# Performance work log

Hardware: AMD Instinct MI355X
Metric: run time of the kernel (lower is better)

## Reference

```python
import jax, jax.numpy as jnp
import numpy as np

B, N, D, P = 4, 512, 512, 128

def setup_inputs() -> dict:
    key = jax.random.key(0)
    ks = jax.random.split(key, 8)
    s = lambda fan_in: 1.0 / np.sqrt(fan_in)
    inp = {
        "input": jax.random.normal(ks[0], (B, N, D), dtype=jnp.float32),
        # bigram projections (weights stored [in, out]; torch Linear is [out, in])
        "Wl": jax.random.uniform(ks[1], (D, P), jnp.float32, -s(D), s(D)),
        "bl": jnp.zeros((P,), jnp.float32),  # zeroed in initialize_parameters
        "Wr": jax.random.uniform(ks[2], (D, P), jnp.float32, -s(D), s(D)),  # no bias
        "Wo": jax.random.uniform(ks[3], (P, 1), jnp.float32, -s(P), s(P)),
        "bo": jnp.zeros((1,), jnp.float32),
        # start builder MLP
        "Ws1": jax.random.uniform(ks[4], (D, P), jnp.float32, -s(D), s(D)),
        "bs1": jnp.zeros((P,), jnp.float32),
        "Ws2": jax.random.uniform(ks[5], (P, 1), jnp.float32, -s(P), s(P)),
        "bs2": jnp.zeros((1,), jnp.float32),
        # end builder MLP
        "We1": jax.random.uniform(ks[6], (D, P), jnp.float32, -s(D), s(D)),
        "be1": jnp.zeros((P,), jnp.float32),
        "We2": jax.random.uniform(ks[7], (P, 1), jnp.float32, -s(P), s(P)),
        "be2": jnp.zeros((1,), jnp.float32),
    }
    return inp


def reference(input, Wl, bl, Wr, Wo, bo, Ws1, bs1, Ws2, bs2, We1, be1, We2, be2):
    # start / end unigram scores: [B, N, 1]
    start = jnp.maximum(input @ Ws1 + bs1, 0.0) @ Ws2 + bs2
    end = jnp.maximum(input @ We1 + be1, 0.0) @ We2 + be2
    # bigram scores
    left = input @ Wl + bl   # [B, N, P]
    right = input @ Wr       # [B, N, P]
    # left.unsqueeze(1) + right.unsqueeze(2) -> [B, N, N, P]
    proj = left[:, None, :, :] + right[:, :, None, :]
    bigram = jnp.maximum(proj, 0.0) @ Wo + bo  # [B, N, N, 1]
    return (bigram, start, end)
```

## Files before the change

### kernel.cpp

```cpp
#include <hip/hip_runtime.h>

typedef unsigned short ushort_t;
using f32x4  = __attribute__((ext_vector_type(4))) float;
using bf16x8 = __attribute__((ext_vector_type(8))) short;
using u16x8  = __attribute__((ext_vector_type(8))) unsigned short;
using h2v    = __attribute__((ext_vector_type(2))) _Float16;
using u32x4  = __attribute__((ext_vector_type(4))) unsigned;

constexpr int Bc = 4;
constexpr int Nc = 512;
constexpr int Dc = 512;
constexpr int Pc = 128;
constexpr int ROWS = Bc * Nc;

__device__ inline unsigned short f2bf(float f) {
    unsigned u = __builtin_bit_cast(unsigned, f);
    unsigned r = u + 0x7fffu + ((u >> 16) & 1u);
    return (unsigned short)(r >> 16);
}

__device__ inline void gload_lds16(const void* g, void* l) {
    __builtin_amdgcn_global_load_lds(
        (const __attribute__((address_space(1))) unsigned int*)g,
        (__attribute__((address_space(3))) unsigned int*)l, 16, 0, 0);
}

__device__ inline unsigned packh2(float a, float b) {
    unsigned short lo = __builtin_bit_cast(unsigned short, (_Float16)a);
    unsigned short hi = __builtin_bit_cast(unsigned short, (_Float16)b);
    return (unsigned)lo | ((unsigned)hi << 16);
}

__global__ __launch_bounds__(256) void wconv_kernel(
    const float* __restrict__ Wl,  const float* __restrict__ Wr,
    const float* __restrict__ Ws1, const float* __restrict__ We1,
    ushort_t* __restrict__ WcatT2)
{
    const int bx = blockIdx.x, t = threadIdx.x;
    __shared__ float T[64][68];

    const int nt = bx >> 3, ks = bx & 7;
    const int mi = nt >> 1, cm0 = (nt & 1) * 64;
    const float* Wm = (mi == 0) ? Wl : (mi == 1) ? Wr : (mi == 2) ? Ws1 : We1;

    const int kk_ = t >> 4, cc = (t & 15) << 2;
    #pragma unroll
    for (int u = 0; u < 4; ++u)
        *(float4*)&T[kk_ + 16 * u][cc] =
            *(const float4*)&Wm[(size_t)(ks * 64 + kk_ + 16 * u) * Pc + cm0 + cc];
    __syncthreads();

    const int col = t & 63, c2 = t >> 6;
    #pragma unroll
    for (int h = 0; h < 2; ++h) {
        const int kc = c2 + h * 4;
        u16x8 o;
        #pragma unroll
        for (int i = 0; i < 8; ++i) o[i] = f2bf(T[kc * 8 + i][col]);
        *(u16x8*)(WcatT2 + ((size_t)(nt * 8 + ks) * 8 + kc) * 512 + col * 8) = o;
    }
}

__global__ __launch_bounds__(256) void mfma_proj4(
    const float* __restrict__ input, const ushort_t* __restrict__ WcatT2,
    const float* __restrict__ bl,
    const float* __restrict__ bs1, const float* __restrict__ Ws2,
    const float* __restrict__ be1, const float* __restrict__ We2,
    ushort_t* __restrict__ leftH, ushort_t* __restrict__ rightH,
    float* __restrict__ parts)
{
    const int mt2 = blockIdx.x, ny = blockIdx.y;
    const int row0 = mt2 * 32;
    const int t = threadIdx.x, w = t >> 6, l = t & 63;
    const int wm = w & 1, wn = w >> 1;
    const int fr = l & 15, fg = l >> 4;

    __shared__ ushort_t As[2][2048];
    __shared__ ushort_t Bs[2][4096];
    __shared__ float red[64];

    const ushort_t* Bbase = WcatT2 + (size_t)ny * 8 * 4096;

    const int sr = t >> 3, skc = t & 7;
    const float* Ain = input + (size_t)(row0 + sr) * Dc + skc * 8;
    ushort_t* Ad0 = &As[0][skc * 256 + sr * 8];
    ushort_t* Ad1 = &As[1][skc * 256 + sr * 8];

    f32x4 acc0 = {0.f, 0.f, 0.f, 0.f}, acc1 = {0.f, 0.f, 0.f, 0.f};
    float4 aE0, aE1, aO0, aO1;

#define ALOAD(P0, P1, KS)                                     \
    {                                                         \
        const float* s_ = Ain + (KS) * 64;                    \
        P0 = *(const float4*)s_;                              \
        P1 = *(const float4*)(s_ + 4);                        \
    }

#define AWRITE(DST, P0, P1)                                   \
    {                                                         \
        u16x8 o_;                                             \
        o_[0] = f2bf(P0.x); o_[1] = f2bf(P0.y);               \
        o_[2] = f2bf(P0.z); o_[3] = f2bf(P0.w);               \
        o_[4] = f2bf(P1.x); o_[5] = f2bf(P1.y);               \
        o_[6] = f2bf(P1.z); o_[7] = f2bf(P1.w);               \
        *(u16x8*)(DST) = o_;                                  \
    }

#define BSTAGE(BI, KS)                                                   \
    {                                                                    \
        const ushort_t* gb = Bbase + (KS) * 4096;                        \
        gload_lds16(gb + w * 512 + l * 8, &Bs[BI][w * 512]);             \
        gload_lds16(gb + (w + 4) * 512 + l * 8, &Bs[BI][(w + 4) * 512]); \
    }

#define COMPUTE(BI)                                                           \
    {                                                                         \
        _Pragma("unroll") for (int kk = 0; kk < 2; ++kk) {                    \
            const int kc = kk * 4 + fg;                                       \
            bf16x8 a  = *(const bf16x8*)&As[BI][kc * 256 + (wm * 16 + fr) * 8];       \
            bf16x8 b0 = *(const bf16x8*)&Bs[BI][kc * 512 + (wn * 32 + fr) * 8];       \
            bf16x8 b1 = *(const bf16x8*)&Bs[BI][kc * 512 + (wn * 32 + 16 + fr) * 8];  \
            acc0 = __builtin_amdgcn_mfma_f32_16x16x32_bf16(a, b0, acc0, 0, 0, 0);     \
            acc1 = __builtin_amdgcn_mfma_f32_16x16x32_bf16(a, b1, acc1, 0, 0, 0);     \
        }                                                                     \
    }

    ALOAD(aE0, aE1, 0);
    BSTAGE(0, 0);
    AWRITE(Ad0, aE0, aE1);
    ALOAD(aO0, aO1, 1);
    __syncthreads();

    #pragma unroll
    for (int ks2 = 0; ks2 < 8; ks2 += 2) {
        BSTAGE(1, ks2 + 1);
        if (ks2 + 2 < 8) ALOAD(aE0, aE1, ks2 + 2);
        COMPUTE(0);
        AWRITE(Ad1, aO0, aO1);
        __syncthreads();
        if (ks2 + 2 < 8) {
            BSTAGE(0, ks2 + 2);
            if (ks2 + 3 < 8) ALOAD(aO0, aO1, ks2 + 3);
        }
        COMPUTE(1);
        if (ks2 + 2 < 8) AWRITE(Ad0, aE0, aE1);
        __syncthreads();
    }
#undef ALOAD
#undef AWRITE
#undef BSTAGE
#undef COMPUTE

    const int fq4 = fg << 2;
    if (ny < 4) {
        ushort_t* outp = (ny < 2) ? leftH : rightH;
        const int cb = (ny & 1) * 64 + wn * 32;
        #pragma unroll
        for (int n = 0; n < 2; ++n) {
            const int col = cb + n * 16 + fr;
            const float bv = (ny < 2) ? bl[col] : 0.f;
            const f32x4 av = n ? acc1 : acc0;
            #pragma unroll
            for (int q = 0; q < 4; ++q) {
                float v = av[q] + bv;
                outp[(size_t)(row0 + wm * 16 + fq4 + q) * Pc + col] =
                    __builtin_bit_cast(ushort_t, (_Float16)v);
            }
        }
    } else {
        const int pi = ny - 4;
        const float* b1 = (ny < 6) ? bs1 : be1;
        const float* W2 = (ny < 6) ? Ws2 : We2;
        const int pb = (pi & 1) * 64;
        #pragma unroll
        for (int q = 0; q < 4; ++q) {
            const int cp0 = pb + wn * 32 + fr;
            const int cp1 = pb + wn * 32 + 16 + fr;
            float v = fmaxf(acc0[q] + b1[cp0], 0.f) * W2[cp0]
                    + fmaxf(acc1[q] + b1[cp1], 0.f) * W2[cp1];
            v += __shfl_xor(v, 1);
            v += __shfl_xor(v, 2);
            v += __shfl_xor(v, 4);
            v += __shfl_xor(v, 8);
            if (fr == 0) red[wn * 32 + wm * 16 + fq4 + q] = v;
        }
        __syncthreads();
        if (t < 32) parts[pi * ROWS + row0 + t] = red[t] + red[32 + t];
    }
}

__global__ __launch_bounds__(256) void bigram_kernel(
    const ushort_t* __restrict__ leftH, const ushort_t* __restrict__ rightH,
    const float* __restrict__ Wo,   const float* __restrict__ bo,
    const float* __restrict__ parts,
    const float* __restrict__ bs2,  const float* __restrict__ be2,
    float* __restrict__ out, float* __restrict__ start_out,
    float* __restrict__ end_out)
{
    const int jt = blockIdx.x, it = blockIdx.y, b = blockIdx.z;
    const int t  = threadIdx.x;

    if (jt == 8) {
        if (it < 8) {
            const int base = (b * 8 + it) * 64;
            if (t < 64) {
                const int r = base + t;
                start_out[r] = parts[r] + parts[ROWS + r] + bs2[0];
            } else if (t < 128) {
                const int r = base + t - 64;
                end_out[r] = parts[2 * ROWS + r] + parts[3 * ROWS + r] + be2[0];
            }
        }
        return;
    }

    __shared__ unsigned Lh[64 * 68];
    __shared__ unsigned Rh[32 * 68];
    __shared__ unsigned woS[64];

    const int lane = t & 63, w = t >> 6;

    if (t < 64) woS[t] = packh2(Wo[2 * t], Wo[2 * t + 1]);

    const ushort_t* lbase = leftH + ((size_t)b * Nc + jt * 64) * Pc;
    #pragma unroll
    for (int u = 0; u < 4; ++u) {
        int idx = t + u * 256, row = idx >> 4, c4 = idx & 15;
        *(u32x4*)&Lh[row * 68 + c4 * 4] =
            *(const u32x4*)(lbase + (size_t)row * Pc + c4 * 8);
    }
    const ushort_t* rbase = rightH + ((size_t)b * Nc + it * 32) * Pc;
    #pragma unroll
    for (int u = 0; u < 2; ++u) {
        int idx = t + u * 256, row = idx >> 4, c4 = idx & 15;
        *(u32x4*)&Rh[row * 68 + c4 * 4] =
            *(const u32x4*)(rbase + (size_t)row * Pc + c4 * 8);
    }
    __syncthreads();

    float acc0[8] = {}, acc1[8] = {};
    const h2v hz = {(_Float16)0.f, (_Float16)0.f};
    const unsigned* lrow = &Lh[lane * 68];
    const unsigned* rw   = &Rh[(w * 8) * 68];

    #pragma unroll
    for (int half = 0; half < 2; ++half) {
        const int hoff = half * 32;

        unsigned lreg[32];
        #pragma unroll
        for (int c = 0; c < 8; ++c) {
            u32x4 v = *(const u32x4*)&lrow[hoff + 4 * c];
            lreg[4 * c]     = v[0]; lreg[4 * c + 1] = v[1];
            lreg[4 * c + 2] = v[2]; lreg[4 * c + 3] = v[3];
        }
        unsigned wreg[32];
        #pragma unroll
        for (int c = 0; c < 8; ++c) {
            u32x4 v = *(const u32x4*)&woS[hoff + 4 * c];
            wreg[4 * c]     = v[0]; wreg[4 * c + 1] = v[1];
            wreg[4 * c + 2] = v[2]; wreg[4 * c + 3] = v[3];
        }

        #pragma unroll
        for (int i = 0; i < 8; ++i) {
            unsigned rreg[32];
            #pragma unroll
            for (int c = 0; c < 8; ++c) {
                u32x4 v = *(const u32x4*)&rw[i * 68 + hoff + 4 * c];
                rreg[4 * c]     = v[0]; rreg[4 * c + 1] = v[1];
                rreg[4 * c + 2] = v[2]; rreg[4 * c + 3] = v[3];
            }
            float a0 = acc0[i], a1 = acc1[i];
            #pragma unroll
            for (int m = 0; m < 32; m += 2) {
                h2v s0 = __builtin_bit_cast(h2v, lreg[m])
                       + __builtin_bit_cast(h2v, rreg[m]);
                s0 = __builtin_elementwise_max(s0, hz);
                a0 = __builtin_amdgcn_fdot2(
                         s0, __builtin_bit_cast(h2v, wreg[m]), a0, false);
                h2v s1 = __builtin_bit_cast(h2v, lreg[m + 1])
                       + __builtin_bit_cast(h2v, rreg[m + 1]);
                s1 = __builtin_elementwise_max(s1, hz);
                a1 = __builtin_amdgcn_fdot2(
                         s1, __builtin_bit_cast(h2v, wreg[m + 1]), a1, false);
            }
            acc0[i] = a0; acc1[i] = a1;
        }
    }

    const float bias = bo[0];
    const int gi0 = it * 32 + w * 8;
    const int gj  = jt * 64 + lane;
    #pragma unroll
    for (int i = 0; i < 8; ++i)
        out[((size_t)b * Nc + gi0 + i) * Nc + gj] = acc0[i] + acc1[i] + bias;
}

extern "C" void kernel_launch(void* const* d_in, const int* in_sizes, int n_in,
                              void* d_out, int out_size, void* d_ws, size_t ws_size,
                              hipStream_t stream) {
    const float* input = (const float*)d_in[0];
    const float* Wl  = (const float*)d_in[1];
    const float* bl  = (const float*)d_in[2];
    const float* Wr  = (const float*)d_in[3];
    const float* Wo  = (const float*)d_in[4];
    const float* bo  = (const float*)d_in[5];
    const float* Ws1 = (const float*)d_in[6];
    const float* bs1 = (const float*)d_in[7];
    const float* Ws2 = (const float*)d_in[8];
    const float* bs2 = (const float*)d_in[9];
    const float* We1 = (const float*)d_in[10];
    const float* be1 = (const float*)d_in[11];
    const float* We2 = (const float*)d_in[12];
    const float* be2 = (const float*)d_in[13];

    float* out    = (float*)d_out;
    float* bigram = out;
    float* start  = out + (size_t)Bc * Nc * Nc;
    float* end    = start + (size_t)Bc * Nc;

    ushort_t* leftH  = (ushort_t*)d_ws;
    ushort_t* rightH = leftH + (size_t)ROWS * Pc;
    float* parts     = (float*)(rightH + (size_t)ROWS * Pc);
    ushort_t* WcatT2 = (ushort_t*)(parts + 4 * ROWS);

    wconv_kernel<<<64, 256, 0, stream>>>(Wl, Wr, Ws1, We1, WcatT2);

    mfma_proj4<<<dim3(64, 8), 256, 0, stream>>>(
        input, WcatT2, bl, bs1, Ws2, be1, We2, leftH, rightH, parts);

    bigram_kernel<<<dim3(9, 16, 4), 256, 0, stream>>>(
        leftH, rightH, Wo, bo, parts, bs2, be2, bigram, start, end);
}
```

Baseline: 31.04 us.

## Replace LDS-tiled bigram kernel with single-wave blocks reading global directly

The bigram kernel no longer stages left/right fp16 rows and Wo in shared memory behind a barrier. It now launches 64-thread blocks with `__launch_bounds__(64, 4)`. Each lane loads its own left row from global and computes 4 output rows, reading the right rows as wave-uniform global loads and packing Wo per thread. This removes LDS traffic and the barrier and gives many more small blocks for scheduling. The cost is that left rows are re-read from cache far more often (128 times instead of 16) and Wo is reloaded by every thread.

```diff
diff --git a/kernel.cpp b/kernel.cpp
--- a/kernel.cpp
+++ b/kernel.cpp
@@ -189,7 +189,7 @@
     }
 }
 
-__global__ __launch_bounds__(256) void bigram_kernel(
+__global__ __launch_bounds__(64, 4) void bigram_kernel(
     const ushort_t* __restrict__ leftH, const ushort_t* __restrict__ rightH,
     const float* __restrict__ Wo,   const float* __restrict__ bo,
     const float* __restrict__ parts,
@@ -197,77 +197,49 @@
     float* __restrict__ out, float* __restrict__ start_out,
     float* __restrict__ end_out)
 {
-    const int jt = blockIdx.x, it = blockIdx.y, b = blockIdx.z;
-    const int t  = threadIdx.x;
-
-    if (jt == 8) {
-        if (it < 8) {
-            const int base = (b * 8 + it) * 64;
-            if (t < 64) {
-                const int r = base + t;
-                start_out[r] = parts[r] + parts[ROWS + r] + bs2[0];
-            } else if (t < 128) {
-                const int r = base + t - 64;
-                end_out[r] = parts[2 * ROWS + r] + parts[3 * ROWS + r] + be2[0];
-            }
+    const int x = blockIdx.x, y = blockIdx.y, b = blockIdx.z;
+    const int t = threadIdx.x;
+
+    if (y == 8) {
+        if (x < 8) {
+            const int r = (b * 8 + x) * 64 + t;
+            start_out[r] = parts[r] + parts[ROWS + r] + bs2[0];
+            end_out[r]   = parts[2 * ROWS + r] + parts[3 * ROWS + r] + be2[0];
         }
         return;
     }
 
-    __shared__ unsigned Lh[64 * 68];
-    __shared__ unsigned Rh[32 * 68];
-    __shared__ unsigned woS[64];
-
-    const int lane = t & 63, w = t >> 6;
-
-    if (t < 64) woS[t] = packh2(Wo[2 * t], Wo[2 * t + 1]);
-
-    const ushort_t* lbase = leftH + ((size_t)b * Nc + jt * 64) * Pc;
-    #pragma unroll
-    for (int u = 0; u < 4; ++u) {
-        int idx = t + u * 256, row = idx >> 4, c4 = idx & 15;
-        *(u32x4*)&Lh[row * 68 + c4 * 4] =
-            *(const u32x4*)(lbase + (size_t)row * Pc + c4 * 8);
-    }
-    const ushort_t* rbase = rightH + ((size_t)b * Nc + it * 32) * Pc;
-    #pragma unroll
-    for (int u = 0; u < 2; ++u) {
-        int idx = t + u * 256, row = idx >> 4, c4 = idx & 15;
-        *(u32x4*)&Rh[row * 68 + c4 * 4] =
-            *(const u32x4*)(rbase + (size_t)row * Pc + c4 * 8);
-    }
-    __syncthreads();
-
-    float acc0[8] = {}, acc1[8] = {};
+    const int j  = y * 64 + t;
+    const int i0 = x * 4;
+
+    const ushort_t* lrow  = leftH  + ((size_t)b * Nc + j) * Pc;
+    const ushort_t* rbase = rightH + ((size_t)b * Nc + i0) * Pc;
+
+    float acc0[4] = {}, acc1[4] = {};
     const h2v hz = {(_Float16)0.f, (_Float16)0.f};
-    const unsigned* lrow = &Lh[lane * 68];
-    const unsigned* rw   = &Rh[(w * 8) * 68];
 
     #pragma unroll
     for (int half = 0; half < 2; ++half) {
-        const int hoff = half * 32;
+        const int hoff = half * 64;
 
         unsigned lreg[32];
         #pragma unroll
         for (int c = 0; c < 8; ++c) {
-            u32x4 v = *(const u32x4*)&lrow[hoff + 4 * c];
+            u32x4 v = *(const u32x4*)(lrow + hoff + c * 8);
             lreg[4 * c]     = v[0]; lreg[4 * c + 1] = v[1];
             lreg[4 * c + 2] = v[2]; lreg[4 * c + 3] = v[3];
         }
         unsigned wreg[32];
         #pragma unroll
-        for (int c = 0; c < 8; ++c) {
-            u32x4 v = *(const u32x4*)&woS[hoff + 4 * c];
-            wreg[4 * c]     = v[0]; wreg[4 * c + 1] = v[1];
-            wreg[4 * c + 2] = v[2]; wreg[4 * c + 3] = v[3];
-        }
-
-        #pragma unroll
-        for (int i = 0; i < 8; ++i) {
+        for (int m = 0; m < 32; ++m)
+            wreg[m] = packh2(Wo[hoff + 2 * m], Wo[hoff + 2 * m + 1]);
+
+        #pragma unroll
+        for (int i = 0; i < 4; ++i) {
             unsigned rreg[32];
             #pragma unroll
             for (int c = 0; c < 8; ++c) {
-                u32x4 v = *(const u32x4*)&rw[i * 68 + hoff + 4 * c];
+                u32x4 v = *(const u32x4*)(rbase + (size_t)i * Pc + hoff + c * 8);
                 rreg[4 * c]     = v[0]; rreg[4 * c + 1] = v[1];
                 rreg[4 * c + 2] = v[2]; rreg[4 * c + 3] = v[3];
             }
@@ -290,11 +262,9 @@
     }
 
     const float bias = bo[0];
-    const int gi0 = it * 32 + w * 8;
-    const int gj  = jt * 64 + lane;
-    #pragma unroll
-    for (int i = 0; i < 8; ++i)
-        out[((size_t)b * Nc + gi0 + i) * Nc + gj] = acc0[i] + acc1[i] + bias;
+    #pragma unroll
+    for (int i = 0; i < 4; ++i)
+        out[((size_t)b * Nc + i0 + i) * Nc + j] = acc0[i] + acc1[i] + bias;
 }
 
 extern "C" void kernel_launch(void* const* d_in, const int* in_sizes, int n_in,
@@ -330,6 +300,6 @@
     mfma_proj4<<<dim3(64, 8), 256, 0, stream>>>(
         input, WcatT2, bl, bs1, Ws2, be1, We2, leftH, rightH, parts);
 
-    bigram_kernel<<<dim3(9, 16, 4), 256, 0, stream>>>(
+    bigram_kernel<<<dim3(128, 9, 4), 64, 0, stream>>>(
         leftH, rightH, Wo, bo, parts, bs2, be2, bigram, start, end);
 }
```

After: 31.20 us (median of 2 runs). No clear change (+0.5%).
